# Kernel optimization log

Measured on AMD Instinct MI355X. Metric: run time of the kernel, lower is better.

The kernel has to match this reference:

```python
import jax, jax.numpy as jnp
import numpy as np

EPS = 1e-5
C = 64  # in_channels == feat_channels == out_channels


def _ln(x, g, b):
    m = jnp.mean(x, axis=-1, keepdims=True)
    v = jnp.mean(jnp.square(x - m), axis=-1, keepdims=True)
    return (x - m) * jax.lax.rsqrt(v + EPS) * g + b


def setup_inputs() -> dict:
    key = jax.random.key(0)
    ks = jax.random.split(key, 10)
    bs, nc, H, W = 8, 80, 256, 256
    d = {
        "feat": jax.random.normal(ks[0], (bs, C, H, W), jnp.float32),
        "head": jax.random.normal(ks[1], (bs, nc, C, 1), jnp.float32),
        "pred": jax.random.normal(ks[2], (bs, nc, H // 2, W // 2), jnp.float32),
        # linear transforms (stored [in, out], applied as x @ W + b)
        "W_pred_t": jax.random.normal(ks[3], (C, 2 * C), jnp.float32) * 0.05,
        "b_pred_t": jnp.zeros((2 * C,), jnp.float32),
        "W_head_t": jax.random.normal(ks[4], (C, 2 * C), jnp.float32) * 0.05,
        "b_head_t": jnp.zeros((2 * C,), jnp.float32),
        "W_pred_g": jax.random.normal(ks[5], (C, C), jnp.float32) * 0.05,
        "b_pred_g": jnp.zeros((C,), jnp.float32),
        "W_head_g": jax.random.normal(ks[6], (C, C), jnp.float32) * 0.05,
        "b_head_g": jnp.zeros((C,), jnp.float32),
        "W_fc": jax.random.normal(ks[7], (C, C), jnp.float32) * 0.05,
        "b_fc": jnp.zeros((C,), jnp.float32),
        # layernorm params
        "g_pin": jnp.ones((C,), jnp.float32), "be_pin": jnp.zeros((C,), jnp.float32),
        "g_hin": jnp.ones((C,), jnp.float32), "be_hin": jnp.zeros((C,), jnp.float32),
        "g_pout": jnp.ones((C,), jnp.float32), "be_pout": jnp.zeros((C,), jnp.float32),
        "g_hout": jnp.ones((C,), jnp.float32), "be_hout": jnp.zeros((C,), jnp.float32),
        "g_fc": jnp.ones((C,), jnp.float32), "be_fc": jnp.zeros((C,), jnp.float32),
    }
    return d


def reference(feat, head, pred,
              W_pred_t, b_pred_t, W_head_t, b_head_t,
              W_pred_g, b_pred_g, W_head_g, b_head_g,
              W_fc, b_fc,
              g_pin, be_pin, g_hin, be_hin,
              g_pout, be_pout, g_hout, be_hout,
              g_fc, be_fc):
    bs, nc = head.shape[:2]
    H, W = feat.shape[2], feat.shape[3]
    pred_up = jax.image.resize(pred, (bs, nc, H, W), method="bilinear")
    pred_up = jax.nn.sigmoid(pred_up)
    # head-aware feature assembly: [bs, nc, C]
    assemble = jnp.einsum("bnhw,bchw->bnc", pred_up, feat)
    a = assemble.reshape(-1, C)                      # [BN, C]
    BN = a.shape[0]
    # head: [bs, nc, C, kk] -> [BN, kk, C]
    hd = jnp.transpose(head.reshape(bs, nc, C, -1), (0, 1, 3, 2)).reshape(BN, -1, C)

    pf = a @ W_pred_t + b_pred_t                     # [BN, 2C]
    pf_in, pf_out = pf[:, :C], pf[:, C:]
    hf = hd @ W_head_t + b_head_t                    # [BN, kk, 2C]
    hf_in, hf_out = hf[..., :C], hf[..., C:]

    gate = hf_in * pf_in[:, None, :]                 # [BN, kk, C]
    head_gate = jax.nn.sigmoid(_ln(gate @ W_head_g + b_head_g, g_hin, be_hin))
    pred_gate = jax.nn.sigmoid(_ln(gate @ W_pred_g + b_pred_g, g_pin, be_pin))

    hf_out = _ln(hf_out, g_hout, be_hout)
    pf_out = _ln(pf_out, g_pout, be_pout)

    upd = pred_gate * pf_out[:, None, :] + head_gate * hf_out
    upd = jax.nn.relu(_ln(upd @ W_fc + b_fc, g_fc, be_fc))
    upd = upd.reshape(bs, nc, -1, C)
    upd = jnp.transpose(upd, (0, 1, 3, 2)).reshape(bs, nc, C, 1, 1)
    return upd
```

## Files before the change

kernel.cpp:

```cpp
#include <hip/hip_runtime.h>
#include <hip/hip_bf16.h>


using bf16x8 = __attribute__((ext_vector_type(8))) short;
using f32x4  = __attribute__((ext_vector_type(4))) float;

__device__ __forceinline__ unsigned pk2(float lo, float hi) {
  union { __hip_bfloat162 h2; unsigned u; } cv;
  cv.h2 = __float22bfloat162_rn(make_float2(lo, hi));
  return cv.u;
}
__device__ __forceinline__ float sigAB(float a, float b) {
  return __builtin_amdgcn_rcpf(1.0f + __builtin_amdgcn_exp2f(-0.36067376f * a - 1.08202128f * b));
}
__device__ __forceinline__ float sigBA(float a, float b) {
  return __builtin_amdgcn_rcpf(1.0f + __builtin_amdgcn_exp2f(-1.08202128f * a - 0.36067376f * b));
}

template<int ROWS>
__global__ __launch_bounds__(256, 3) void k_assemble(
    const float* __restrict__ feat, const float* __restrict__ pred,
    float* __restrict__ partial) {
  __shared__ __align__(16) unsigned short Pfrag[40 * 64 * 8];

  constexpr int LOGN = (ROWS == 2) ? 7 : 6;
  const int tid = threadIdx.x;
  const int b  = blockIdx.x >> LOGN;
  const int rb = blockIdx.x & ((1 << LOGN) - 1);
  const int wid = tid >> 6, l = tid & 63;
  const int ch16 = l & 15, kg = l >> 4;
  const int c0 = wid << 4;
  const int h0 = rb * ROWS;
  const int gg = tid & 31, nb = tid >> 5;

  f32x4 acc[5] = {};
  const float* fwave = feat + (((size_t)(b * 64 + c0 + ch16)) << 16);
  const float* pbat  = pred + (((size_t)(b * 80)) << 14);

  #pragma unroll
  for (int r = 0; r < ROWS; ++r) {
    const int h = h0 + r;
    const int j = h >> 1;
    int r0, r1; float wy0, wy1;
    if ((h & 1) == 0) { r0 = (j > 0) ? j - 1 : 0; r1 = j; wy0 = 0.25f; wy1 = 0.75f; }
    else              { r0 = j; r1 = (j < 127) ? j + 1 : 127; wy0 = 0.75f; wy1 = 0.25f; }

    float y[10][4];
    #pragma unroll
    for (int i = 0; i < 10; ++i) {
      const int n = nb + 8 * i;
      const float* pb = pbat + (((size_t)n) << 14);
      const float4 v0 = *(const float4*)(pb + (r0 << 7) + gg * 4);
      const float4 v1 = *(const float4*)(pb + (r1 << 7) + gg * 4);
      y[i][0] = wy0 * v0.x + wy1 * v1.x; y[i][1] = wy0 * v0.y + wy1 * v1.y;
      y[i][2] = wy0 * v0.z + wy1 * v1.z; y[i][3] = wy0 * v0.w + wy1 * v1.w;
    }

    const float* fb = fwave + h * 256;
    float4 f[16];
    #pragma unroll
    for (int ks = 0; ks < 8; ++ks) {
      const int pw = ks * 32 + kg * 8;
      f[2 * ks]     = *(const float4*)(fb + pw);
      f[2 * ks + 1] = *(const float4*)(fb + pw + 4);
    }

    #pragma unroll
    for (int i = 0; i < 10; ++i) {
      const int n = nb + 8 * i;
      const float y0 = y[i][0], y1 = y[i][1], y2 = y[i][2], y3 = y[i][3];
      float yl = __shfl_up(y3, 1, 64);   if (gg == 0)  yl = y0;
      float yr = __shfl_down(y0, 1, 64); if (gg == 31) yr = y3;
      float P[8];
      P[0] = sigAB(yl, y0); P[1] = sigBA(y0, y1);
      P[2] = sigAB(y0, y1); P[3] = sigBA(y1, y2);
      P[4] = sigAB(y1, y2); P[5] = sigBA(y2, y3);
      P[6] = sigAB(y2, y3); P[7] = sigBA(y3, yr);
      uint4 s;
      s.x = pk2(P[0], P[1]); s.y = pk2(P[2], P[3]);
      s.z = pk2(P[4], P[5]); s.w = pk2(P[6], P[7]);
      const int ks = gg >> 2, kgw = gg & 3;
      const int slot = kgw * 16 + ((n & 15) ^ ks);
      *(uint4*)&Pfrag[(((ks * 5 + (n >> 4)) * 64) + slot) * 8] = s;
    }
    asm volatile("s_waitcnt lgkmcnt(0)" ::: "memory");
    __builtin_amdgcn_s_barrier();

    #pragma unroll
    for (int ks = 0; ks < 8; ++ks) {
      const float4 f0 = f[2 * ks], f1 = f[2 * ks + 1];
      union { uint4 u; bf16x8 v; } bu;
      bu.u.x = pk2(f0.x, f0.y); bu.u.y = pk2(f0.z, f0.w);
      bu.u.z = pk2(f1.x, f1.y); bu.u.w = pk2(f1.z, f1.w);
      const int slot = kg * 16 + (ch16 ^ ks);
      #pragma unroll
      for (int m = 0; m < 5; ++m) {
        const bf16x8 af = *(const bf16x8*)&Pfrag[(((ks * 5 + m) * 64) + slot) * 8];
        acc[m] = __builtin_amdgcn_mfma_f32_16x16x32_bf16(af, bu.v, acc[m], 0, 0, 0);
      }
    }
    asm volatile("s_waitcnt lgkmcnt(0)" ::: "memory");
    __builtin_amdgcn_s_barrier();
  }

  float* po = partial + ((size_t)((b << LOGN) + rb)) * (80 * 64);
  #pragma unroll
  for (int m = 0; m < 5; ++m) {
    #pragma unroll
    for (int q = 0; q < 4; ++q) {
      const int n = m * 16 + kg * 4 + q;
      po[n * 64 + c0 + ch16] = acc[m][q];
    }
  }
}

__device__ __forceinline__ float wred64(float v) {
  #pragma unroll
  for (int off = 32; off > 0; off >>= 1) v += __shfl_xor(v, off, 64);
  return v;
}
__device__ __forceinline__ float lnorm(float x, const float* __restrict__ g,
                                       const float* __restrict__ be, int l) {
  const float m = wred64(x) * 0.015625f;
  const float d = x - m;
  const float var = wred64(d * d) * 0.015625f;
  return d * rsqrtf(var + 1e-5f) * g[l] + be[l];
}
__device__ __forceinline__ float sigmf(float x) {
  return __builtin_amdgcn_rcpf(1.0f + __builtin_amdgcn_exp2f(-1.44269504f * x));
}

__global__ __launch_bounds__(256) void k_head(
    const float* __restrict__ partial, const float* __restrict__ head,
    const float* __restrict__ Wpt, const float* __restrict__ bpt,
    const float* __restrict__ Wht, const float* __restrict__ bht,
    const float* __restrict__ Wpg, const float* __restrict__ bpg,
    const float* __restrict__ Whg, const float* __restrict__ bhg,
    const float* __restrict__ Wfc, const float* __restrict__ bfc,
    const float* __restrict__ g_pin, const float* __restrict__ be_pin,
    const float* __restrict__ g_hin, const float* __restrict__ be_hin,
    const float* __restrict__ g_pout, const float* __restrict__ be_pout,
    const float* __restrict__ g_hout, const float* __restrict__ be_hout,
    const float* __restrict__ g_fc, const float* __restrict__ be_fc,
    float* __restrict__ out, int npart) {
  __shared__ float red[4][64];
  __shared__ float buf[4][64];
  const int tid = threadIdx.x, c = tid & 63, q = tid >> 6;
  const int r = blockIdx.x;
  const int b = r / 80, n = r % 80;
  const int npq = npart >> 2;

  const float* pp = partial + ((size_t)b * npart + (size_t)q * npq) * 5120 + n * 64 + c;
  float s = 0.f;
  #pragma unroll 8
  for (int jj = 0; jj < npq; ++jj) s += pp[(size_t)jj * 5120];
  red[q][c] = s;
  __syncthreads();

  if (q == 0) {
    const float a_c = red[0][c] + red[1][c] + red[2][c] + red[3][c];
    buf[0][c] = a_c;
    buf[1][c] = head[(size_t)r * 64 + c];

    float pf_in = bpt[c], pf_out = bpt[64 + c];
    float hf_in = bht[c], hf_out = bht[64 + c];
    #pragma unroll 8
    for (int k = 0; k < 64; ++k) {
      const float av = buf[0][k];
      const float hv = buf[1][k];
      pf_in  += av * Wpt[k * 128 + c];
      pf_out += av * Wpt[k * 128 + 64 + c];
      hf_in  += hv * Wht[k * 128 + c];
      hf_out += hv * Wht[k * 128 + 64 + c];
    }
    buf[2][c] = hf_in * pf_in;

    float hg = bhg[c], pg = bpg[c];
    #pragma unroll 8
    for (int k = 0; k < 64; ++k) {
      const float gv = buf[2][k];
      hg += gv * Whg[k * 64 + c];
      pg += gv * Wpg[k * 64 + c];
    }
    const float head_gate = sigmf(lnorm(hg, g_hin, be_hin, c));
    const float pred_gate = sigmf(lnorm(pg, g_pin, be_pin, c));
    const float hfo = lnorm(hf_out, g_hout, be_hout, c);
    const float pfo = lnorm(pf_out, g_pout, be_pout, c);
    buf[3][c] = pred_gate * pfo + head_gate * hfo;

    float fc = bfc[c];
    #pragma unroll 8
    for (int k = 0; k < 64; ++k)
      fc += buf[3][k] * Wfc[k * 64 + c];
    float o = lnorm(fc, g_fc, be_fc, c);
    out[(size_t)r * 64 + c] = fmaxf(o, 0.f);
  }
}

extern "C" void kernel_launch(void* const* d_in, const int* in_sizes, int n_in,
                              void* d_out, int out_size, void* d_ws, size_t ws_size,
                              hipStream_t stream) {
  const float* feat   = (const float*)d_in[0];
  const float* head   = (const float*)d_in[1];
  const float* pred   = (const float*)d_in[2];
  const float* Wpt    = (const float*)d_in[3];
  const float* bpt    = (const float*)d_in[4];
  const float* Wht    = (const float*)d_in[5];
  const float* bht    = (const float*)d_in[6];
  const float* Wpg    = (const float*)d_in[7];
  const float* bpg    = (const float*)d_in[8];
  const float* Whg    = (const float*)d_in[9];
  const float* bhg    = (const float*)d_in[10];
  const float* Wfc    = (const float*)d_in[11];
  const float* bfc    = (const float*)d_in[12];
  const float* g_pin  = (const float*)d_in[13];
  const float* be_pin = (const float*)d_in[14];
  const float* g_hin  = (const float*)d_in[15];
  const float* be_hin = (const float*)d_in[16];
  const float* g_pout = (const float*)d_in[17];
  const float* be_pout= (const float*)d_in[18];
  const float* g_hout = (const float*)d_in[19];
  const float* be_hout= (const float*)d_in[20];
  const float* g_fc   = (const float*)d_in[21];
  const float* be_fc  = (const float*)d_in[22];
  float* out = (float*)d_out;
  float* partial = (float*)d_ws;

  const bool big = ws_size >= (size_t)8 * 128 * 5120 * 4;
  const int npart = big ? 128 : 64;

  if (big)
    hipLaunchKernelGGL((k_assemble<2>), dim3(8 * 128), dim3(256), 0, stream,
                       feat, pred, partial);
  else
    hipLaunchKernelGGL((k_assemble<4>), dim3(8 * 64), dim3(256), 0, stream,
                       feat, pred, partial);

  hipLaunchKernelGGL(k_head, dim3(640), dim3(256), 0, stream,
                     partial, head, Wpt, bpt, Wht, bht, Wpg, bpg, Whg, bhg,
                     Wfc, bfc, g_pin, be_pin, g_hin, be_hin, g_pout, be_pout,
                     g_hout, be_hout, g_fc, be_fc, out, npart);
}
```

Before: 65.46 us.

## Software-pipeline feat and pred row loads with inline-asm prefetch and double buffering

Result: no change. 64.70 us (-1.2%).

```diff
diff --git a/kernel.cpp b/kernel.cpp
--- a/kernel.cpp
+++ b/kernel.cpp
@@ -4,6 +4,18 @@
 
 using bf16x8 = __attribute__((ext_vector_type(8))) short;
 using f32x4  = __attribute__((ext_vector_type(4))) float;
+
+#define NPART 64
+#define ROWS 4
+
+#define GLD4(dst, ptr) \
+  asm volatile("global_load_dwordx4 %0, %1, off" : "=v"(dst) : "v"(ptr) : "memory")
+#define WAITV(n) do { \
+  asm volatile("s_waitcnt vmcnt(" #n ")" ::: "memory"); \
+  __builtin_amdgcn_sched_barrier(0); } while (0)
+#define LGKM_BARRIER() do { \
+  asm volatile("s_waitcnt lgkmcnt(0)" ::: "memory"); \
+  __builtin_amdgcn_s_barrier(); } while (0)
 
 __device__ __forceinline__ unsigned pk2(float lo, float hi) {
   union { __hip_bfloat162 h2; unsigned u; } cv;
@@ -17,16 +29,86 @@
   return __builtin_amdgcn_rcpf(1.0f + __builtin_amdgcn_exp2f(-1.08202128f * a - 0.36067376f * b));
 }
 
-template<int ROWS>
-__global__ __launch_bounds__(256, 3) void k_assemble(
+template<int R>
+__device__ __forceinline__ void row_body(
+    const float* __restrict__ fwave, const float* __restrict__ pbat,
+    unsigned short* Pfrag, int h0, int gg, int nb, int ch16, int kg,
+    f32x4 (&FCUR)[16], f32x4 (&FNXT)[16],
+    f32x4 (&p0)[10], f32x4 (&p1)[10], f32x4 (&acc)[5]) {
+  const int h = h0 + R;
+  constexpr float wy0 = (R & 1) ? 0.75f : 0.25f;
+  constexpr float wy1 = (R & 1) ? 0.25f : 0.75f;
+
+  WAITV(16);
+
+  #pragma unroll
+  for (int i = 0; i < 10; ++i) {
+    const int n = nb + 8 * i;
+    const float y0 = wy0 * p0[i][0] + wy1 * p1[i][0];
+    const float y1 = wy0 * p0[i][1] + wy1 * p1[i][1];
+    const float y2 = wy0 * p0[i][2] + wy1 * p1[i][2];
+    const float y3 = wy0 * p0[i][3] + wy1 * p1[i][3];
+    float yl = __shfl_up(y3, 1, 64);   if (gg == 0)  yl = y0;
+    float yr = __shfl_down(y0, 1, 64); if (gg == 31) yr = y3;
+    float P[8];
+    P[0] = sigAB(yl, y0); P[1] = sigBA(y0, y1);
+    P[2] = sigAB(y0, y1); P[3] = sigBA(y1, y2);
+    P[4] = sigAB(y1, y2); P[5] = sigBA(y2, y3);
+    P[6] = sigAB(y2, y3); P[7] = sigBA(y3, yr);
+    uint4 s;
+    s.x = pk2(P[0], P[1]); s.y = pk2(P[2], P[3]);
+    s.z = pk2(P[4], P[5]); s.w = pk2(P[6], P[7]);
+    const int ks = gg >> 2, kgw = gg & 3;
+    const int slot = kgw * 16 + ((n & 15) ^ ks);
+    *(uint4*)&Pfrag[(((ks * 5 + (n >> 4)) * 64) + slot) * 8] = s;
+  }
+  LGKM_BARRIER();
+
+  if constexpr (R < ROWS - 1) {
+    const int hn = h + 1;
+    const int j = hn >> 1;
+    int r0_, r1_;
+    if ((hn & 1) == 0) { r0_ = (j > 0) ? j - 1 : 0; r1_ = j; }
+    else               { r0_ = j; r1_ = (j < 127) ? j + 1 : 127; }
+    #pragma unroll
+    for (int i = 0; i < 10; ++i) {
+      const float* pb = pbat + (((size_t)(nb + 8 * i)) << 14);
+      GLD4(p0[i], pb + (r0_ << 7) + gg * 4);
+      GLD4(p1[i], pb + (r1_ << 7) + gg * 4);
+    }
+  }
+
+  if constexpr (R == ROWS - 1) { WAITV(0); }
+  const float* fbn = fwave + (h + 1) * 256;
+  #pragma unroll
+  for (int ks = 0; ks < 8; ++ks) {
+    if constexpr (R < ROWS - 1) { WAITV(34); }
+    const f32x4 f0 = FCUR[2 * ks], f1 = FCUR[2 * ks + 1];
+    union { uint4 u; bf16x8 v; } bu;
+    bu.u.x = pk2(f0[0], f0[1]); bu.u.y = pk2(f0[2], f0[3]);
+    bu.u.z = pk2(f1[0], f1[1]); bu.u.w = pk2(f1[2], f1[3]);
+    if constexpr (R < ROWS - 1) {
+      GLD4(FNXT[2 * ks],     fbn + ks * 32 + kg * 8);
+      GLD4(FNXT[2 * ks + 1], fbn + ks * 32 + kg * 8 + 4);
+    }
+    const int slot = kg * 16 + (ch16 ^ ks);
+    #pragma unroll
+    for (int m = 0; m < 5; ++m) {
+      const bf16x8 af = *(const bf16x8*)&Pfrag[(((ks * 5 + m) * 64) + slot) * 8];
+      acc[m] = __builtin_amdgcn_mfma_f32_16x16x32_bf16(af, bu.v, acc[m], 0, 0, 0);
+    }
+  }
+  LGKM_BARRIER();
+}
+
+__global__ __launch_bounds__(256, 2) void k_assemble(
     const float* __restrict__ feat, const float* __restrict__ pred,
     float* __restrict__ partial) {
   __shared__ __align__(16) unsigned short Pfrag[40 * 64 * 8];
 
-  constexpr int LOGN = (ROWS == 2) ? 7 : 6;
   const int tid = threadIdx.x;
-  const int b  = blockIdx.x >> LOGN;
-  const int rb = blockIdx.x & ((1 << LOGN) - 1);
+  const int b  = blockIdx.x >> 6;
+  const int rb = blockIdx.x & 63;
   const int wid = tid >> 6, l = tid & 63;
   const int ch16 = l & 15, kg = l >> 4;
   const int c0 = wid << 4;
@@ -37,73 +119,32 @@
   const float* fwave = feat + (((size_t)(b * 64 + c0 + ch16)) << 16);
   const float* pbat  = pred + (((size_t)(b * 80)) << 14);
 
-  #pragma unroll
-  for (int r = 0; r < ROWS; ++r) {
-    const int h = h0 + r;
-    const int j = h >> 1;
-    int r0, r1; float wy0, wy1;
-    if ((h & 1) == 0) { r0 = (j > 0) ? j - 1 : 0; r1 = j; wy0 = 0.25f; wy1 = 0.75f; }
-    else              { r0 = j; r1 = (j < 127) ? j + 1 : 127; wy0 = 0.75f; wy1 = 0.25f; }
-
-    float y[10][4];
+  f32x4 p0[10], p1[10];
+  f32x4 fA[16], fB[16];
+
+  {
+    const int j = h0 >> 1;
+    const int r0_ = (j > 0) ? j - 1 : 0, r1_ = j;
     #pragma unroll
     for (int i = 0; i < 10; ++i) {
-      const int n = nb + 8 * i;
-      const float* pb = pbat + (((size_t)n) << 14);
-      const float4 v0 = *(const float4*)(pb + (r0 << 7) + gg * 4);
-      const float4 v1 = *(const float4*)(pb + (r1 << 7) + gg * 4);
-      y[i][0] = wy0 * v0.x + wy1 * v1.x; y[i][1] = wy0 * v0.y + wy1 * v1.y;
-      y[i][2] = wy0 * v0.z + wy1 * v1.z; y[i][3] = wy0 * v0.w + wy1 * v1.w;
-    }
-
-    const float* fb = fwave + h * 256;
-    float4 f[16];
+      const float* pb = pbat + (((size_t)(nb + 8 * i)) << 14);
+      GLD4(p0[i], pb + (r0_ << 7) + gg * 4);
+      GLD4(p1[i], pb + (r1_ << 7) + gg * 4);
+    }
+    const float* fb = fwave + h0 * 256;
     #pragma unroll
     for (int ks = 0; ks < 8; ++ks) {
-      const int pw = ks * 32 + kg * 8;
-      f[2 * ks]     = *(const float4*)(fb + pw);
-      f[2 * ks + 1] = *(const float4*)(fb + pw + 4);
-    }
-
-    #pragma unroll
-    for (int i = 0; i < 10; ++i) {
-      const int n = nb + 8 * i;
-      const float y0 = y[i][0], y1 = y[i][1], y2 = y[i][2], y3 = y[i][3];
-      float yl = __shfl_up(y3, 1, 64);   if (gg == 0)  yl = y0;
-      float yr = __shfl_down(y0, 1, 64); if (gg == 31) yr = y3;
-      float P[8];
-      P[0] = sigAB(yl, y0); P[1] = sigBA(y0, y1);
-      P[2] = sigAB(y0, y1); P[3] = sigBA(y1, y2);
-      P[4] = sigAB(y1, y2); P[5] = sigBA(y2, y3);
-      P[6] = sigAB(y2, y3); P[7] = sigBA(y3, yr);
-      uint4 s;
-      s.x = pk2(P[0], P[1]); s.y = pk2(P[2], P[3]);
-      s.z = pk2(P[4], P[5]); s.w = pk2(P[6], P[7]);
-      const int ks = gg >> 2, kgw = gg & 3;
-      const int slot = kgw * 16 + ((n & 15) ^ ks);
-      *(uint4*)&Pfrag[(((ks * 5 + (n >> 4)) * 64) + slot) * 8] = s;
-    }
-    asm volatile("s_waitcnt lgkmcnt(0)" ::: "memory");
-    __builtin_amdgcn_s_barrier();
-
-    #pragma unroll
-    for (int ks = 0; ks < 8; ++ks) {
-      const float4 f0 = f[2 * ks], f1 = f[2 * ks + 1];
-      union { uint4 u; bf16x8 v; } bu;
-      bu.u.x = pk2(f0.x, f0.y); bu.u.y = pk2(f0.z, f0.w);
-      bu.u.z = pk2(f1.x, f1.y); bu.u.w = pk2(f1.z, f1.w);
-      const int slot = kg * 16 + (ch16 ^ ks);
-      #pragma unroll
-      for (int m = 0; m < 5; ++m) {
-        const bf16x8 af = *(const bf16x8*)&Pfrag[(((ks * 5 + m) * 64) + slot) * 8];
-        acc[m] = __builtin_amdgcn_mfma_f32_16x16x32_bf16(af, bu.v, acc[m], 0, 0, 0);
-      }
-    }
-    asm volatile("s_waitcnt lgkmcnt(0)" ::: "memory");
-    __builtin_amdgcn_s_barrier();
-  }
-
-  float* po = partial + ((size_t)((b << LOGN) + rb)) * (80 * 64);
+      GLD4(fA[2 * ks],     fb + ks * 32 + kg * 8);
+      GLD4(fA[2 * ks + 1], fb + ks * 32 + kg * 8 + 4);
+    }
+  }
+
+  row_body<0>(fwave, pbat, Pfrag, h0, gg, nb, ch16, kg, fA, fB, p0, p1, acc);
+  row_body<1>(fwave, pbat, Pfrag, h0, gg, nb, ch16, kg, fB, fA, p0, p1, acc);
+  row_body<2>(fwave, pbat, Pfrag, h0, gg, nb, ch16, kg, fA, fB, p0, p1, acc);
+  row_body<3>(fwave, pbat, Pfrag, h0, gg, nb, ch16, kg, fB, fA, p0, p1, acc);
+
+  float* po = partial + ((size_t)(b * NPART + rb)) * (80 * 64);
   #pragma unroll
   for (int m = 0; m < 5; ++m) {
     #pragma unroll
@@ -226,18 +267,10 @@
   float* out = (float*)d_out;
   float* partial = (float*)d_ws;
 
-  const bool big = ws_size >= (size_t)8 * 128 * 5120 * 4;
-  const int npart = big ? 128 : 64;
-
-  if (big)
-    hipLaunchKernelGGL((k_assemble<2>), dim3(8 * 128), dim3(256), 0, stream,
-                       feat, pred, partial);
-  else
-    hipLaunchKernelGGL((k_assemble<4>), dim3(8 * 64), dim3(256), 0, stream,
-                       feat, pred, partial);
-
+  hipLaunchKernelGGL(k_assemble, dim3(8 * NPART), dim3(256), 0, stream,
+                     feat, pred, partial);
   hipLaunchKernelGGL(k_head, dim3(640), dim3(256), 0, stream,
                      partial, head, Wpt, bpt, Wht, bht, Wpg, bpg, Whg, bhg,
                      Wfc, bfc, g_pin, be_pin, g_hin, be_hin, g_pout, be_pout,
-                     g_hout, be_hout, g_fc, be_fc, out, npart);
-}
+                     g_hout, be_hout, g_fc, be_fc, out, NPART);
+}
```
